# Kernel optimization log

Measured on AMD Instinct MI355X. Metric: run time of the kernel, lower is better.

The kernel has to match this reference:

```python
import jax, jax.numpy as jnp
import numpy as np

B, D = 16384, 1024
H1, H2 = 512, 256
T = 3          # num_tasks
E_SH = 2       # num_shared_experts
E_SP = 2       # num_specific_experts
G = E_SH + E_SP


def setup_inputs() -> dict:
    key = jax.random.key(0)
    ks = jax.random.split(key, 8)
    def glorot(k, shape, fan_in, fan_out):
        return jax.random.normal(k, shape, jnp.float32) * jnp.sqrt(2.0 / (fan_in + fan_out))
    return {
        "x": jax.random.normal(ks[0], (B, D), jnp.float32),
        "shared_W1": glorot(ks[1], (E_SH, D, H1), D, H1),
        "shared_b1": jnp.zeros((E_SH, H1), jnp.float32),
        "shared_W2": glorot(ks[2], (E_SH, H1, H2), H1, H2),
        "shared_b2": jnp.zeros((E_SH, H2), jnp.float32),
        "spec_W1": glorot(ks[3], (T, E_SP, D, H1), D, H1),
        "spec_b1": jnp.zeros((T, E_SP, H1), jnp.float32),
        "spec_W2": glorot(ks[4], (T, E_SP, H1, H2), H1, H2),
        "spec_b2": jnp.zeros((T, E_SP, H2), jnp.float32),
        "gate_W": glorot(ks[5], (T, D, G), D, G),
        "gate_b": jnp.zeros((T, G), jnp.float32),
    }


def reference(x, shared_W1, shared_b1, shared_W2, shared_b2,
              spec_W1, spec_b1, spec_W2, spec_b2, gate_W, gate_b):
    # Shared experts: two-layer MLP with relu, batched over experts. [B, E_SH, H2]
    sh = jax.nn.relu(jnp.einsum('bi,eih->beh', x, shared_W1) + shared_b1)
    sh = jax.nn.relu(jnp.einsum('beh,eho->beo', sh, shared_W2) + shared_b2)
    # Task-specific experts, batched over (task, expert). [B, T, E_SP, H2]
    sp = jax.nn.relu(jnp.einsum('bi,teih->bteh', x, spec_W1) + spec_b1)
    sp = jax.nn.relu(jnp.einsum('bteh,teho->bteo', sp, spec_W2) + spec_b2)
    # Gates: single linear layer per task + softmax over G=E_SH+E_SP experts. [B, T, G]
    gate = jax.nn.softmax(jnp.einsum('bi,tig->btg', x, gate_W) + gate_b, axis=-1)
    # Experts stacked in order: shared first, then specific (matches tf.stack order).
    sh_b = jnp.broadcast_to(sh[:, None], (B, T, E_SH, H2))
    experts = jnp.concatenate([sh_b, sp], axis=2)  # [B, T, G, H2]
    # Gate-weighted sum over the expert axis -> per-task outputs [B, T, H2]
    out = jnp.einsum('btgh,btg->bth', experts, gate)
    return out
```

## Files before the change

### kernel.cpp

```cpp
#include <hip/hip_runtime.h>
#include <hip/hip_bf16.h>
#include <stdint.h>

#define B_SZ 16384
#define D_SZ 1024
#define H1_SZ 512
#define H2_SZ 256
#define T_SZ 3
#define ESH 2
#define NE 8

typedef __bf16 bf16x8 __attribute__((ext_vector_type(8)));
typedef float f32x4 __attribute__((ext_vector_type(4)));
typedef unsigned short u16;
typedef u16 u16x8 __attribute__((ext_vector_type(8)));

__device__ __forceinline__ u16 f2bf(float f) {
  union { float f; uint32_t u; } v; v.f = f;
  uint32_t u = v.u;
  uint32_t r = (u + 0x7FFFu + ((u >> 16) & 1u)) >> 16;
  return (u16)r;
}
__device__ __forceinline__ float bf2f(u16 b) {
  union { uint32_t u; float f; } v; v.u = ((uint32_t)b) << 16;
  return v.f;
}

__device__ __forceinline__ void gload16(const u16* src, u16* dst_lds) {
  __builtin_amdgcn_global_load_lds(
      (const __attribute__((address_space(1))) void*)src,
      (__attribute__((address_space(3))) void*)dst_lds, 16, 0, 0);
}

__global__ __launch_bounds__(256) void cast_f32_to_bf16(
    const float* __restrict__ in, u16* __restrict__ out, int n8) {
  int i = blockIdx.x * blockDim.x + threadIdx.x;
  if (i >= n8) return;
  const float4* p = (const float4*)in + (size_t)i * 2;
  float4 a = p[0], b = p[1];
  u16x8 o;
  o[0] = f2bf(a.x); o[1] = f2bf(a.y); o[2] = f2bf(a.z); o[3] = f2bf(a.w);
  o[4] = f2bf(b.x); o[5] = f2bf(b.y); o[6] = f2bf(b.z); o[7] = f2bf(b.w);
  *((u16x8*)out + i) = o;
}

__global__ __launch_bounds__(256) void transpose_cast(
    const float* __restrict__ src, u16* __restrict__ dst, int K, int N) {
  __shared__ float tile[32][33];
  size_t e = blockIdx.z;
  const float* s = src + e * (size_t)K * N;
  u16* d = dst + e * (size_t)K * N;
  int n0 = blockIdx.x * 32, k0 = blockIdx.y * 32;
  int tx = threadIdx.x, ty = threadIdx.y;
#pragma unroll
  for (int i = ty; i < 32; i += 8)
    tile[i][tx] = s[(size_t)(k0 + i) * N + n0 + tx];
  __syncthreads();
#pragma unroll
  for (int i = ty; i < 32; i += 8)
    d[(size_t)(n0 + i) * K + k0 + tx] = f2bf(tile[tx][i]);
}

__global__ __launch_bounds__(256, 2) void gemm_ring3(
    const u16* __restrict__ A, size_t strideAe,
    const u16* __restrict__ Bt,
    const float* __restrict__ bias_sh, const float* __restrict__ bias_sp,
    u16* __restrict__ C, int M, int N, int K, int ntn_sh) {
  __shared__ __align__(16) u16 lds[3 * 12288];
  const int tid = threadIdx.x;
  const int wid = tid >> 6, lane = tid & 63;
  const int fr = lane & 15, fq = lane >> 4;
  const int wc = wid;

  const int bid = blockIdx.x;
  const int e = bid & 7;
  const int r = bid >> 3;
  const int mtile = r >> ntn_sh;
  const int ntile = r & ((1 << ntn_sh) - 1);
  const int m0 = mtile * 128, n0 = ntile * 256;

  const u16* Ae = A + (size_t)e * strideAe;
  const u16* Be = Bt + (size_t)e * (size_t)N * K;
  const int NT = K >> 5;

  const u16* pA[2];
  const u16* pB[4];
#pragma unroll
  for (int p = 0; p < 2; ++p) {
    int c = p * 256 + tid, row = c >> 2, sl = (c & 3) ^ ((row >> 1) & 3);
    pA[p] = Ae + (size_t)(m0 + row) * K + sl * 8;
  }
#pragma unroll
  for (int p = 0; p < 4; ++p) {
    int c = p * 256 + tid, row = c >> 2, sl = (c & 3) ^ ((row >> 1) & 3);
    pB[p] = Be + (size_t)(n0 + row) * K + sl * 8;
  }
  const int wdst = wid * 512;

  int offA[8], offB[4];
#pragma unroll
  for (int m = 0; m < 8; ++m) {
    int rr = m * 16 + fr;
    offA[m] = rr * 32 + ((fq ^ ((rr >> 1) & 3)) * 8);
  }
#pragma unroll
  for (int n = 0; n < 4; ++n) {
    int cg = wc * 64 + n * 16 + fr;
    offB[n] = 4096 + cg * 32 + ((fq ^ ((cg >> 1) & 3)) * 8);
  }

  f32x4 acc[8][4] = {};

#define STAGE(t, sb) do {                                             \
    gload16(pA[0] + (size_t)(t) * 32, &lds[(sb) + wdst]);             \
    gload16(pA[1] + (size_t)(t) * 32, &lds[(sb) + 2048 + wdst]);      \
    gload16(pB[0] + (size_t)(t) * 32, &lds[(sb) + 4096 + wdst]);      \
    gload16(pB[1] + (size_t)(t) * 32, &lds[(sb) + 6144 + wdst]);      \
    gload16(pB[2] + (size_t)(t) * 32, &lds[(sb) + 8192 + wdst]);      \
    gload16(pB[3] + (size_t)(t) * 32, &lds[(sb) + 10240 + wdst]); } while (0)

  STAGE(0, 0);
  STAGE(1, 12288);
  asm volatile("s_waitcnt vmcnt(6)");
  __builtin_amdgcn_s_barrier();
  __builtin_amdgcn_sched_barrier(0);

  int sb_cur = 0;
  for (int t = 0; t < NT; ++t) {
    const u16* sl = &lds[sb_cur];
    bf16x8 av[8], bv[4];
#pragma unroll
    for (int m = 0; m < 8; ++m) av[m] = *(const bf16x8*)&sl[offA[m]];
#pragma unroll
    for (int n = 0; n < 4; ++n) bv[n] = *(const bf16x8*)&sl[offB[n]];
    if (t + 2 < NT) {
      int sb_n2 = sb_cur + 2 * 12288;
      if (sb_n2 >= 36864) sb_n2 -= 36864;
      STAGE(t + 2, sb_n2);
    }
    __builtin_amdgcn_s_setprio(1);
#pragma unroll
    for (int m = 0; m < 8; ++m)
#pragma unroll
      for (int n = 0; n < 4; ++n)
        acc[m][n] = __builtin_amdgcn_mfma_f32_16x16x32_bf16(av[m], bv[n], acc[m][n], 0, 0, 0);
    __builtin_amdgcn_s_setprio(0);
    if (t + 2 < NT)      asm volatile("s_waitcnt vmcnt(6)");
    else if (t + 1 < NT) asm volatile("s_waitcnt vmcnt(0)");
    __builtin_amdgcn_s_barrier();
    __builtin_amdgcn_sched_barrier(0);
    sb_cur += 12288;
    if (sb_cur >= 36864) sb_cur = 0;
  }
#undef STAGE

  const float* bias = (e < ESH) ? (bias_sh + (size_t)e * N)
                                : (bias_sp + (size_t)(e - ESH) * N);
  u16* Ce = C + (size_t)e * (size_t)M * N;
  float bb[4];
#pragma unroll
  for (int n = 0; n < 4; ++n) bb[n] = bias[n0 + wc * 64 + n * 16 + fr];

#pragma unroll
  for (int m = 0; m < 8; ++m) {
#pragma unroll
    for (int n = 0; n < 4; ++n) {
      const int col = wc * 64 + n * 16 + fr;
      f32x4 a = acc[m][n];
#pragma unroll
      for (int rr = 0; rr < 4; ++rr) {
        float v = a[rr] + bb[n];
        v = v > 0.f ? v : 0.f;
        lds[(m * 16 + fq * 4 + rr) * 264 + col] = f2bf(v);
      }
    }
  }
  __builtin_amdgcn_s_barrier();
  const int cc = (tid & 31) * 8;
  const int rr8 = tid >> 5;
#pragma unroll
  for (int pass = 0; pass < 16; ++pass) {
    const int lr = pass * 8 + rr8;
    u16x8 vv = *(const u16x8*)&lds[lr * 264 + cc];
    *(u16x8*)&Ce[(size_t)(m0 + lr) * N + n0 + cc] = vv;
  }
}

__global__ __launch_bounds__(256) void gates_kernel(
    const float* __restrict__ x, const float* __restrict__ gW,
    const float* __restrict__ gb, float* __restrict__ gates) {
  __shared__ float gw[12][1024];
  const int tid = threadIdx.x;
  for (int i = tid; i < 12 * 1024; i += 256) {
    int tg = i >> 10, k = i & 1023;
    gw[tg][k] = gW[(size_t)(tg >> 2) * 4096 + (size_t)k * 4 + (tg & 3)];
  }
  __syncthreads();
  const int wid = tid >> 6, lane = tid & 63;
  const size_t b = (size_t)blockIdx.x * 4 + wid;
  const float* xr = x + b * 1024;
  float acc[12] = {};
  for (int kk = 0; kk < 16; ++kk) {
    float xv = xr[kk * 64 + lane];
#pragma unroll
    for (int t = 0; t < 12; ++t) acc[t] += xv * gw[t][kk * 64 + lane];
  }
#pragma unroll
  for (int off = 32; off >= 1; off >>= 1)
#pragma unroll
    for (int t = 0; t < 12; ++t) acc[t] += __shfl_xor(acc[t], off);
  if (lane == 0) {
    float* gr = gates + b * 12;
#pragma unroll
    for (int t = 0; t < 3; ++t) {
      float l0 = acc[t * 4 + 0] + gb[t * 4 + 0];
      float l1 = acc[t * 4 + 1] + gb[t * 4 + 1];
      float l2 = acc[t * 4 + 2] + gb[t * 4 + 2];
      float l3 = acc[t * 4 + 3] + gb[t * 4 + 3];
      float mx = fmaxf(fmaxf(l0, l1), fmaxf(l2, l3));
      float e0 = __expf(l0 - mx), e1 = __expf(l1 - mx);
      float e2 = __expf(l2 - mx), e3 = __expf(l3 - mx);
      float inv = 1.f / (e0 + e1 + e2 + e3);
      gr[t * 4 + 0] = e0 * inv; gr[t * 4 + 1] = e1 * inv;
      gr[t * 4 + 2] = e2 * inv; gr[t * 4 + 3] = e3 * inv;
    }
  }
}

__global__ __launch_bounds__(256) void combine_kernel(
    const u16* __restrict__ y2, const float* __restrict__ gates,
    float* __restrict__ out) {
  const int tid = threadIdx.x;
  const int rb = tid >> 5;
  const int hc = (tid & 31) * 8;
  const size_t b = (size_t)blockIdx.x * 8 + rb;
  const float* g = gates + b * 12;
  float acc0[8] = {}, acc1[8] = {}, acc2[8] = {};
#pragma unroll
  for (int e = 0; e < 8; ++e) {
    u16x8 v = *(const u16x8*)&y2[(size_t)e * B_SZ * H2_SZ + b * H2_SZ + hc];
    float f[8];
#pragma unroll
    for (int i = 0; i < 8; ++i) f[i] = bf2f(v[i]);
    if (e < 2) {
      float g0 = g[0 * 4 + e], g1 = g[1 * 4 + e], g2 = g[2 * 4 + e];
#pragma unroll
      for (int i = 0; i < 8; ++i) {
        acc0[i] += g0 * f[i]; acc1[i] += g1 * f[i]; acc2[i] += g2 * f[i];
      }
    } else {
      const int t = (e - 2) >> 1, gi = 2 + ((e - 2) & 1);
      float gv = g[t * 4 + gi];
      float* acc = (t == 0) ? acc0 : (t == 1) ? acc1 : acc2;
#pragma unroll
      for (int i = 0; i < 8; ++i) acc[i] += gv * f[i];
    }
  }
  float* o = out + b * (3 * 256);
  *(float4*)&o[0 * 256 + hc]     = make_float4(acc0[0], acc0[1], acc0[2], acc0[3]);
  *(float4*)&o[0 * 256 + hc + 4] = make_float4(acc0[4], acc0[5], acc0[6], acc0[7]);
  *(float4*)&o[1 * 256 + hc]     = make_float4(acc1[0], acc1[1], acc1[2], acc1[3]);
  *(float4*)&o[1 * 256 + hc + 4] = make_float4(acc1[4], acc1[5], acc1[6], acc1[7]);
  *(float4*)&o[2 * 256 + hc]     = make_float4(acc2[0], acc2[1], acc2[2], acc2[3]);
  *(float4*)&o[2 * 256 + hc + 4] = make_float4(acc2[4], acc2[5], acc2[6], acc2[7]);
}

extern "C" void kernel_launch(void* const* d_in, const int* in_sizes, int n_in,
                              void* d_out, int out_size, void* d_ws, size_t ws_size,
                              hipStream_t stream) {
  (void)in_sizes; (void)n_in; (void)out_size; (void)ws_size;
  const float* x   = (const float*)d_in[0];
  const float* sW1 = (const float*)d_in[1];
  const float* sb1 = (const float*)d_in[2];
  const float* sW2 = (const float*)d_in[3];
  const float* sb2 = (const float*)d_in[4];
  const float* pW1 = (const float*)d_in[5];
  const float* pb1 = (const float*)d_in[6];
  const float* pW2 = (const float*)d_in[7];
  const float* pb2 = (const float*)d_in[8];
  const float* gW  = (const float*)d_in[9];
  const float* gb  = (const float*)d_in[10];

  uint8_t* ws = (uint8_t*)d_ws;
  u16* xb    = (u16*)(ws);
  u16* w1t   = (u16*)(ws + 33554432);
  u16* w2t   = (u16*)(ws + 41943040);
  u16* y1    = (u16*)(ws + 44040192);
  u16* y2    = (u16*)(ws + 178257920);
  float* gts = (float*)(ws + 245366784);

  cast_f32_to_bf16<<<(B_SZ * D_SZ / 8 + 255) / 256, 256, 0, stream>>>(
      x, xb, B_SZ * D_SZ / 8);

  transpose_cast<<<dim3(512 / 32, 1024 / 32, 2), dim3(32, 8), 0, stream>>>(
      sW1, w1t, 1024, 512);
  transpose_cast<<<dim3(512 / 32, 1024 / 32, 6), dim3(32, 8), 0, stream>>>(
      pW1, w1t + (size_t)2 * 1024 * 512, 1024, 512);
  transpose_cast<<<dim3(256 / 32, 512 / 32, 2), dim3(32, 8), 0, stream>>>(
      sW2, w2t, 512, 256);
  transpose_cast<<<dim3(256 / 32, 512 / 32, 6), dim3(32, 8), 0, stream>>>(
      pW2, w2t + (size_t)2 * 512 * 256, 512, 256);

  gates_kernel<<<B_SZ / 4, 256, 0, stream>>>(x, gW, gb, gts);

  gemm_ring3<<<(B_SZ / 128) * (512 / 256) * NE, 256, 0, stream>>>(
      xb, 0, w1t, sb1, pb1, y1, B_SZ, 512, 1024, 1);

  gemm_ring3<<<(B_SZ / 128) * (256 / 256) * NE, 256, 0, stream>>>(
      y1, (size_t)B_SZ * 512, w2t, sb2, pb2, y2, B_SZ, 256, 512, 0);

  combine_kernel<<<B_SZ / 8, 256, 0, stream>>>(y2, gts, (float*)d_out);
}
```

Baseline: 309.1 us.

## Fuse layer-2 GEMM with gated combine; merge casts into gates and transpose kernels

Replaces the second expert GEMM and the combine kernel with a single kernel. It loops over all 8 experts for a 64x128 output tile, applies bias and ReLU, and accumulates the gate-weighted sum in registers. This avoids writing the bf16 y2 intermediate to memory and reading it back. It also folds the x cast into the gates kernel and merges the four weight transposes into one launch. The cost is fewer blocks (512) with smaller tiles, a serial loop over experts, and a large register footprint for the per-task accumulators.

```diff
diff --git a/kernel.cpp b/kernel.cpp
--- a/kernel.cpp
+++ b/kernel.cpp
@@ -32,24 +32,26 @@
       (__attribute__((address_space(3))) void*)dst_lds, 16, 0, 0);
 }
 
-__global__ __launch_bounds__(256) void cast_f32_to_bf16(
-    const float* __restrict__ in, u16* __restrict__ out, int n8) {
-  int i = blockIdx.x * blockDim.x + threadIdx.x;
-  if (i >= n8) return;
-  const float4* p = (const float4*)in + (size_t)i * 2;
-  float4 a = p[0], b = p[1];
-  u16x8 o;
-  o[0] = f2bf(a.x); o[1] = f2bf(a.y); o[2] = f2bf(a.z); o[3] = f2bf(a.w);
-  o[4] = f2bf(b.x); o[5] = f2bf(b.y); o[6] = f2bf(b.z); o[7] = f2bf(b.w);
-  *((u16x8*)out + i) = o;
-}
-
-__global__ __launch_bounds__(256) void transpose_cast(
-    const float* __restrict__ src, u16* __restrict__ dst, int K, int N) {
+__global__ __launch_bounds__(256) void transpose_cast_all(
+    const float* __restrict__ sW1, const float* __restrict__ pW1,
+    const float* __restrict__ sW2, const float* __restrict__ pW2,
+    u16* __restrict__ w1t, u16* __restrict__ w2t) {
   __shared__ float tile[32][33];
-  size_t e = blockIdx.z;
-  const float* s = src + e * (size_t)K * N;
-  u16* d = dst + e * (size_t)K * N;
+  const int z = blockIdx.z;
+  int K, N;
+  const float* s;
+  u16* d;
+  if (z < 8) {
+    K = 1024; N = 512;
+    s = (z < 2) ? (sW1 + (size_t)z * K * N) : (pW1 + (size_t)(z - 2) * K * N);
+    d = w1t + (size_t)z * K * N;
+  } else {
+    K = 512; N = 256;
+    const int e = z - 8;
+    if (blockIdx.x >= 8 || blockIdx.y >= 16) return;
+    s = (e < 2) ? (sW2 + (size_t)e * K * N) : (pW2 + (size_t)(e - 2) * K * N);
+    d = w2t + (size_t)e * K * N;
+  }
   int n0 = blockIdx.x * 32, k0 = blockIdx.y * 32;
   int tx = threadIdx.x, ty = threadIdx.y;
 #pragma unroll
@@ -61,134 +63,10 @@
     d[(size_t)(n0 + i) * K + k0 + tx] = f2bf(tile[tx][i]);
 }
 
-__global__ __launch_bounds__(256, 2) void gemm_ring3(
-    const u16* __restrict__ A, size_t strideAe,
-    const u16* __restrict__ Bt,
-    const float* __restrict__ bias_sh, const float* __restrict__ bias_sp,
-    u16* __restrict__ C, int M, int N, int K, int ntn_sh) {
-  __shared__ __align__(16) u16 lds[3 * 12288];
-  const int tid = threadIdx.x;
-  const int wid = tid >> 6, lane = tid & 63;
-  const int fr = lane & 15, fq = lane >> 4;
-  const int wc = wid;
-
-  const int bid = blockIdx.x;
-  const int e = bid & 7;
-  const int r = bid >> 3;
-  const int mtile = r >> ntn_sh;
-  const int ntile = r & ((1 << ntn_sh) - 1);
-  const int m0 = mtile * 128, n0 = ntile * 256;
-
-  const u16* Ae = A + (size_t)e * strideAe;
-  const u16* Be = Bt + (size_t)e * (size_t)N * K;
-  const int NT = K >> 5;
-
-  const u16* pA[2];
-  const u16* pB[4];
-#pragma unroll
-  for (int p = 0; p < 2; ++p) {
-    int c = p * 256 + tid, row = c >> 2, sl = (c & 3) ^ ((row >> 1) & 3);
-    pA[p] = Ae + (size_t)(m0 + row) * K + sl * 8;
-  }
-#pragma unroll
-  for (int p = 0; p < 4; ++p) {
-    int c = p * 256 + tid, row = c >> 2, sl = (c & 3) ^ ((row >> 1) & 3);
-    pB[p] = Be + (size_t)(n0 + row) * K + sl * 8;
-  }
-  const int wdst = wid * 512;
-
-  int offA[8], offB[4];
-#pragma unroll
-  for (int m = 0; m < 8; ++m) {
-    int rr = m * 16 + fr;
-    offA[m] = rr * 32 + ((fq ^ ((rr >> 1) & 3)) * 8);
-  }
-#pragma unroll
-  for (int n = 0; n < 4; ++n) {
-    int cg = wc * 64 + n * 16 + fr;
-    offB[n] = 4096 + cg * 32 + ((fq ^ ((cg >> 1) & 3)) * 8);
-  }
-
-  f32x4 acc[8][4] = {};
-
-#define STAGE(t, sb) do {                                             \
-    gload16(pA[0] + (size_t)(t) * 32, &lds[(sb) + wdst]);             \
-    gload16(pA[1] + (size_t)(t) * 32, &lds[(sb) + 2048 + wdst]);      \
-    gload16(pB[0] + (size_t)(t) * 32, &lds[(sb) + 4096 + wdst]);      \
-    gload16(pB[1] + (size_t)(t) * 32, &lds[(sb) + 6144 + wdst]);      \
-    gload16(pB[2] + (size_t)(t) * 32, &lds[(sb) + 8192 + wdst]);      \
-    gload16(pB[3] + (size_t)(t) * 32, &lds[(sb) + 10240 + wdst]); } while (0)
-
-  STAGE(0, 0);
-  STAGE(1, 12288);
-  asm volatile("s_waitcnt vmcnt(6)");
-  __builtin_amdgcn_s_barrier();
-  __builtin_amdgcn_sched_barrier(0);
-
-  int sb_cur = 0;
-  for (int t = 0; t < NT; ++t) {
-    const u16* sl = &lds[sb_cur];
-    bf16x8 av[8], bv[4];
-#pragma unroll
-    for (int m = 0; m < 8; ++m) av[m] = *(const bf16x8*)&sl[offA[m]];
-#pragma unroll
-    for (int n = 0; n < 4; ++n) bv[n] = *(const bf16x8*)&sl[offB[n]];
-    if (t + 2 < NT) {
-      int sb_n2 = sb_cur + 2 * 12288;
-      if (sb_n2 >= 36864) sb_n2 -= 36864;
-      STAGE(t + 2, sb_n2);
-    }
-    __builtin_amdgcn_s_setprio(1);
-#pragma unroll
-    for (int m = 0; m < 8; ++m)
-#pragma unroll
-      for (int n = 0; n < 4; ++n)
-        acc[m][n] = __builtin_amdgcn_mfma_f32_16x16x32_bf16(av[m], bv[n], acc[m][n], 0, 0, 0);
-    __builtin_amdgcn_s_setprio(0);
-    if (t + 2 < NT)      asm volatile("s_waitcnt vmcnt(6)");
-    else if (t + 1 < NT) asm volatile("s_waitcnt vmcnt(0)");
-    __builtin_amdgcn_s_barrier();
-    __builtin_amdgcn_sched_barrier(0);
-    sb_cur += 12288;
-    if (sb_cur >= 36864) sb_cur = 0;
-  }
-#undef STAGE
-
-  const float* bias = (e < ESH) ? (bias_sh + (size_t)e * N)
-                                : (bias_sp + (size_t)(e - ESH) * N);
-  u16* Ce = C + (size_t)e * (size_t)M * N;
-  float bb[4];
-#pragma unroll
-  for (int n = 0; n < 4; ++n) bb[n] = bias[n0 + wc * 64 + n * 16 + fr];
-
-#pragma unroll
-  for (int m = 0; m < 8; ++m) {
-#pragma unroll
-    for (int n = 0; n < 4; ++n) {
-      const int col = wc * 64 + n * 16 + fr;
-      f32x4 a = acc[m][n];
-#pragma unroll
-      for (int rr = 0; rr < 4; ++rr) {
-        float v = a[rr] + bb[n];
-        v = v > 0.f ? v : 0.f;
-        lds[(m * 16 + fq * 4 + rr) * 264 + col] = f2bf(v);
-      }
-    }
-  }
-  __builtin_amdgcn_s_barrier();
-  const int cc = (tid & 31) * 8;
-  const int rr8 = tid >> 5;
-#pragma unroll
-  for (int pass = 0; pass < 16; ++pass) {
-    const int lr = pass * 8 + rr8;
-    u16x8 vv = *(const u16x8*)&lds[lr * 264 + cc];
-    *(u16x8*)&Ce[(size_t)(m0 + lr) * N + n0 + cc] = vv;
-  }
-}
-
-__global__ __launch_bounds__(256) void gates_kernel(
+__global__ __launch_bounds__(256) void gates_cast_kernel(
     const float* __restrict__ x, const float* __restrict__ gW,
-    const float* __restrict__ gb, float* __restrict__ gates) {
+    const float* __restrict__ gb, float* __restrict__ gates,
+    u16* __restrict__ xb) {
   __shared__ float gw[12][1024];
   const int tid = threadIdx.x;
   for (int i = tid; i < 12 * 1024; i += 256) {
@@ -199,9 +77,11 @@
   const int wid = tid >> 6, lane = tid & 63;
   const size_t b = (size_t)blockIdx.x * 4 + wid;
   const float* xr = x + b * 1024;
+  u16* xbr = xb + b * 1024;
   float acc[12] = {};
   for (int kk = 0; kk < 16; ++kk) {
     float xv = xr[kk * 64 + lane];
+    xbr[kk * 64 + lane] = f2bf(xv);
 #pragma unroll
     for (int t = 0; t < 12; ++t) acc[t] += xv * gw[t][kk * 64 + lane];
   }
@@ -227,42 +107,271 @@
   }
 }
 
-__global__ __launch_bounds__(256) void combine_kernel(
-    const u16* __restrict__ y2, const float* __restrict__ gates,
-    float* __restrict__ out) {
+__global__ __launch_bounds__(256, 2) void gemm_ring3(
+    const u16* __restrict__ A, size_t strideAe,
+    const u16* __restrict__ Bt,
+    const float* __restrict__ bias_sh, const float* __restrict__ bias_sp,
+    u16* __restrict__ C, int M, int N, int K, int ntn_sh) {
+  __shared__ __align__(16) u16 lds[3 * 12288];
   const int tid = threadIdx.x;
-  const int rb = tid >> 5;
-  const int hc = (tid & 31) * 8;
-  const size_t b = (size_t)blockIdx.x * 8 + rb;
-  const float* g = gates + b * 12;
-  float acc0[8] = {}, acc1[8] = {}, acc2[8] = {};
-#pragma unroll
-  for (int e = 0; e < 8; ++e) {
-    u16x8 v = *(const u16x8*)&y2[(size_t)e * B_SZ * H2_SZ + b * H2_SZ + hc];
-    float f[8];
-#pragma unroll
-    for (int i = 0; i < 8; ++i) f[i] = bf2f(v[i]);
-    if (e < 2) {
-      float g0 = g[0 * 4 + e], g1 = g[1 * 4 + e], g2 = g[2 * 4 + e];
-#pragma unroll
-      for (int i = 0; i < 8; ++i) {
-        acc0[i] += g0 * f[i]; acc1[i] += g1 * f[i]; acc2[i] += g2 * f[i];
+  const int wid = tid >> 6, lane = tid & 63;
+  const int fr = lane & 15, fq = lane >> 4;
+  const int wc = wid;
+
+  const int bid = blockIdx.x;
+  const int e = bid & 7;
+  const int r = bid >> 3;
+  const int mtile = r >> ntn_sh;
+  const int ntile = r & ((1 << ntn_sh) - 1);
+  const int m0 = mtile * 128, n0 = ntile * 256;
+
+  const u16* Ae = A + (size_t)e * strideAe;
+  const u16* Be = Bt + (size_t)e * (size_t)N * K;
+  const int NT = K >> 5;
+
+  const u16* pA[2];
+  const u16* pB[4];
+#pragma unroll
+  for (int p = 0; p < 2; ++p) {
+    int c = p * 256 + tid, row = c >> 2, sl = (c & 3) ^ ((row >> 1) & 3);
+    pA[p] = Ae + (size_t)(m0 + row) * K + sl * 8;
+  }
+#pragma unroll
+  for (int p = 0; p < 4; ++p) {
+    int c = p * 256 + tid, row = c >> 2, sl = (c & 3) ^ ((row >> 1) & 3);
+    pB[p] = Be + (size_t)(n0 + row) * K + sl * 8;
+  }
+  const int wdst = wid * 512;
+
+  int offA[8], offB[4];
+#pragma unroll
+  for (int m = 0; m < 8; ++m) {
+    int rr = m * 16 + fr;
+    offA[m] = rr * 32 + ((fq ^ ((rr >> 1) & 3)) * 8);
+  }
+#pragma unroll
+  for (int n = 0; n < 4; ++n) {
+    int cg = wc * 64 + n * 16 + fr;
+    offB[n] = 4096 + cg * 32 + ((fq ^ ((cg >> 1) & 3)) * 8);
+  }
+
+  f32x4 acc[8][4] = {};
+
+#define STAGE(t, sb) do {                                             \
+    gload16(pA[0] + (size_t)(t) * 32, &lds[(sb) + wdst]);             \
+    gload16(pA[1] + (size_t)(t) * 32, &lds[(sb) + 2048 + wdst]);      \
+    gload16(pB[0] + (size_t)(t) * 32, &lds[(sb) + 4096 + wdst]);      \
+    gload16(pB[1] + (size_t)(t) * 32, &lds[(sb) + 6144 + wdst]);      \
+    gload16(pB[2] + (size_t)(t) * 32, &lds[(sb) + 8192 + wdst]);      \
+    gload16(pB[3] + (size_t)(t) * 32, &lds[(sb) + 10240 + wdst]); } while (0)
+
+  STAGE(0, 0);
+  STAGE(1, 12288);
+  asm volatile("s_waitcnt vmcnt(6)");
+  __builtin_amdgcn_s_barrier();
+  __builtin_amdgcn_sched_barrier(0);
+
+  int sb_cur = 0;
+  for (int t = 0; t < NT; ++t) {
+    const u16* sl = &lds[sb_cur];
+    bf16x8 av[8], bv[4];
+#pragma unroll
+    for (int m = 0; m < 8; ++m) av[m] = *(const bf16x8*)&sl[offA[m]];
+#pragma unroll
+    for (int n = 0; n < 4; ++n) bv[n] = *(const bf16x8*)&sl[offB[n]];
+    if (t + 2 < NT) {
+      int sb_n2 = sb_cur + 2 * 12288;
+      if (sb_n2 >= 36864) sb_n2 -= 36864;
+      STAGE(t + 2, sb_n2);
+    }
+    __builtin_amdgcn_s_setprio(1);
+#pragma unroll
+    for (int m = 0; m < 8; ++m)
+#pragma unroll
+      for (int n = 0; n < 4; ++n)
+        acc[m][n] = __builtin_amdgcn_mfma_f32_16x16x32_bf16(av[m], bv[n], acc[m][n], 0, 0, 0);
+    __builtin_amdgcn_s_setprio(0);
+    if (t + 2 < NT)      asm volatile("s_waitcnt vmcnt(6)");
+    else if (t + 1 < NT) asm volatile("s_waitcnt vmcnt(0)");
+    __builtin_amdgcn_s_barrier();
+    __builtin_amdgcn_sched_barrier(0);
+    sb_cur += 12288;
+    if (sb_cur >= 36864) sb_cur = 0;
+  }
+#undef STAGE
+
+  const float* bias = (e < ESH) ? (bias_sh + (size_t)e * N)
+                                : (bias_sp + (size_t)(e - ESH) * N);
+  u16* Ce = C + (size_t)e * (size_t)M * N;
+  float bb[4];
+#pragma unroll
+  for (int n = 0; n < 4; ++n) bb[n] = bias[n0 + wc * 64 + n * 16 + fr];
+
+#pragma unroll
+  for (int m = 0; m < 8; ++m) {
+#pragma unroll
+    for (int n = 0; n < 4; ++n) {
+      const int col = wc * 64 + n * 16 + fr;
+      f32x4 a = acc[m][n];
+#pragma unroll
+      for (int rr = 0; rr < 4; ++rr) {
+        float v = a[rr] + bb[n];
+        v = v > 0.f ? v : 0.f;
+        lds[(m * 16 + fq * 4 + rr) * 264 + col] = f2bf(v);
       }
-    } else {
-      const int t = (e - 2) >> 1, gi = 2 + ((e - 2) & 1);
-      float gv = g[t * 4 + gi];
-      float* acc = (t == 0) ? acc0 : (t == 1) ? acc1 : acc2;
-#pragma unroll
-      for (int i = 0; i < 8; ++i) acc[i] += gv * f[i];
     }
   }
-  float* o = out + b * (3 * 256);
-  *(float4*)&o[0 * 256 + hc]     = make_float4(acc0[0], acc0[1], acc0[2], acc0[3]);
-  *(float4*)&o[0 * 256 + hc + 4] = make_float4(acc0[4], acc0[5], acc0[6], acc0[7]);
-  *(float4*)&o[1 * 256 + hc]     = make_float4(acc1[0], acc1[1], acc1[2], acc1[3]);
-  *(float4*)&o[1 * 256 + hc + 4] = make_float4(acc1[4], acc1[5], acc1[6], acc1[7]);
-  *(float4*)&o[2 * 256 + hc]     = make_float4(acc2[0], acc2[1], acc2[2], acc2[3]);
-  *(float4*)&o[2 * 256 + hc + 4] = make_float4(acc2[4], acc2[5], acc2[6], acc2[7]);
+  __builtin_amdgcn_s_barrier();
+  const int cc = (tid & 31) * 8;
+  const int rr8 = tid >> 5;
+#pragma unroll
+  for (int pass = 0; pass < 16; ++pass) {
+    const int lr = pass * 8 + rr8;
+    u16x8 vv = *(const u16x8*)&lds[lr * 264 + cc];
+    *(u16x8*)&Ce[(size_t)(m0 + lr) * N + n0 + cc] = vv;
+  }
+}
+
+__global__ __launch_bounds__(256, 2) void fused_l2c(
+    const u16* __restrict__ y1, const u16* __restrict__ w2t,
+    const float* __restrict__ sb2, const float* __restrict__ pb2,
+    const float* __restrict__ gts, float* __restrict__ out) {
+  __shared__ __align__(16) u16 ring[3 * 6144];
+  __shared__ float gl[64 * 12];
+  __shared__ float bl[8 * 128];
+  const int tid = threadIdx.x;
+  const int wid = tid >> 6, lane = tid & 63;
+  const int fr = lane & 15, fq = lane >> 4;
+
+  const int bid = blockIdx.x;
+  const int bm = bid >> 1, bn = bid & 1;
+  const int m0 = bm * 64;
+  const int ncol0 = bn * 128;
+
+  for (int i = tid; i < 768; i += 256)
+    gl[i] = gts[(size_t)(m0 + i / 12) * 12 + (i % 12)];
+  for (int i = tid; i < 1024; i += 256) {
+    int e = i >> 7, c = i & 127;
+    bl[i] = (e < 2) ? sb2[e * 256 + ncol0 + c] : pb2[(e - 2) * 256 + ncol0 + c];
+  }
+
+  const int cA = tid, rowA = cA >> 2, slA = (cA & 3) ^ ((rowA >> 1) & 3);
+  const u16* pAf = y1 + (size_t)(m0 + rowA) * 512 + slA * 8;
+  const u16* pBf[2];
+#pragma unroll
+  for (int p = 0; p < 2; ++p) {
+    int c = p * 256 + tid, row = c >> 2, sl = (c & 3) ^ ((row >> 1) & 3);
+    pBf[p] = w2t + (size_t)(ncol0 + row) * 512 + sl * 8;
+  }
+  const int wdst = wid * 512;
+
+  int offA[4], offB[2];
+#pragma unroll
+  for (int m = 0; m < 4; ++m) {
+    int rr = m * 16 + fr;
+    offA[m] = rr * 32 + ((fq ^ ((rr >> 1) & 3)) * 8);
+  }
+#pragma unroll
+  for (int n = 0; n < 2; ++n) {
+    int cg = wid * 32 + n * 16 + fr;
+    offB[n] = 2048 + cg * 32 + ((fq ^ ((cg >> 1) & 3)) * 8);
+  }
+
+  f32x4 acc[4][2] = {};
+  float oa[3][4][2][4] = {};
+
+#define STAGE2(g, sb) do {                                                      \
+    const size_t eo = (size_t)((g) >> 4);                                       \
+    const int ko = ((g) & 15) * 32;                                             \
+    gload16(pAf + eo * ((size_t)B_SZ * 512) + ko, &ring[(sb) + wdst]);          \
+    gload16(pBf[0] + eo * 131072 + ko, &ring[(sb) + 2048 + wdst]);              \
+    gload16(pBf[1] + eo * 131072 + ko, &ring[(sb) + 4096 + wdst]); } while (0)
+
+  STAGE2(0, 0);
+  STAGE2(1, 6144);
+  __syncthreads();
+
+  int sb_cur = 0;
+  for (int g = 0; g < 128; ++g) {
+    const u16* sl = &ring[sb_cur];
+    bf16x8 av[4], bv[2];
+#pragma unroll
+    for (int m = 0; m < 4; ++m) av[m] = *(const bf16x8*)&sl[offA[m]];
+#pragma unroll
+    for (int n = 0; n < 2; ++n) bv[n] = *(const bf16x8*)&sl[offB[n]];
+    if (g + 2 < 128) {
+      int sb_n2 = sb_cur + 2 * 6144;
+      if (sb_n2 >= 18432) sb_n2 -= 18432;
+      STAGE2(g + 2, sb_n2);
+    }
+    __builtin_amdgcn_s_setprio(1);
+#pragma unroll
+    for (int m = 0; m < 4; ++m)
+#pragma unroll
+      for (int n = 0; n < 2; ++n)
+        acc[m][n] = __builtin_amdgcn_mfma_f32_16x16x32_bf16(av[m], bv[n], acc[m][n], 0, 0, 0);
+    __builtin_amdgcn_s_setprio(0);
+    if (g + 2 < 128)      asm volatile("s_waitcnt vmcnt(3)");
+    else if (g + 1 < 128) asm volatile("s_waitcnt vmcnt(0)");
+    __builtin_amdgcn_s_barrier();
+    __builtin_amdgcn_sched_barrier(0);
+    sb_cur += 6144;
+    if (sb_cur >= 18432) sb_cur = 0;
+
+    if ((g & 15) == 15) {
+      const int e = g >> 4;
+#pragma unroll
+      for (int m = 0; m < 4; ++m) {
+#pragma unroll
+        for (int rr = 0; rr < 4; ++rr) {
+          const int row = m * 16 + fq * 4 + rr;
+          if (e < 2) {
+            const float g0 = gl[row * 12 + 0 * 4 + e];
+            const float g1 = gl[row * 12 + 1 * 4 + e];
+            const float g2 = gl[row * 12 + 2 * 4 + e];
+#pragma unroll
+            for (int n = 0; n < 2; ++n) {
+              const int col = wid * 32 + n * 16 + fr;
+              float v = acc[m][n][rr] + bl[e * 128 + col];
+              v = v > 0.f ? v : 0.f;
+              oa[0][m][n][rr] += g0 * v;
+              oa[1][m][n][rr] += g1 * v;
+              oa[2][m][n][rr] += g2 * v;
+            }
+          } else {
+            const int t = (e - 2) >> 1, gi = 2 + ((e - 2) & 1);
+            const float gv = gl[row * 12 + t * 4 + gi];
+#pragma unroll
+            for (int n = 0; n < 2; ++n) {
+              const int col = wid * 32 + n * 16 + fr;
+              float v = acc[m][n][rr] + bl[e * 128 + col];
+              v = v > 0.f ? v : 0.f;
+              if (t == 0) oa[0][m][n][rr] += gv * v;
+              else if (t == 1) oa[1][m][n][rr] += gv * v;
+              else oa[2][m][n][rr] += gv * v;
+            }
+          }
+#pragma unroll
+          for (int n = 0; n < 2; ++n) acc[m][n][rr] = 0.f;
+        }
+      }
+    }
+  }
+#undef STAGE2
+
+#pragma unroll
+  for (int t = 0; t < 3; ++t)
+#pragma unroll
+    for (int m = 0; m < 4; ++m)
+#pragma unroll
+      for (int rr = 0; rr < 4; ++rr) {
+        const int row = m * 16 + fq * 4 + rr;
+#pragma unroll
+        for (int n = 0; n < 2; ++n) {
+          const int col = wid * 32 + n * 16 + fr;
+          out[(size_t)(m0 + row) * 768 + t * 256 + ncol0 + col] = oa[t][m][n][rr];
+        }
+      }
 }
 
 extern "C" void kernel_launch(void* const* d_in, const int* in_sizes, int n_in,
@@ -286,28 +395,16 @@
   u16* w1t   = (u16*)(ws + 33554432);
   u16* w2t   = (u16*)(ws + 41943040);
   u16* y1    = (u16*)(ws + 44040192);
-  u16* y2    = (u16*)(ws + 178257920);
-  float* gts = (float*)(ws + 245366784);
-
-  cast_f32_to_bf16<<<(B_SZ * D_SZ / 8 + 255) / 256, 256, 0, stream>>>(
-      x, xb, B_SZ * D_SZ / 8);
-
-  transpose_cast<<<dim3(512 / 32, 1024 / 32, 2), dim3(32, 8), 0, stream>>>(
-      sW1, w1t, 1024, 512);
-  transpose_cast<<<dim3(512 / 32, 1024 / 32, 6), dim3(32, 8), 0, stream>>>(
-      pW1, w1t + (size_t)2 * 1024 * 512, 1024, 512);
-  transpose_cast<<<dim3(256 / 32, 512 / 32, 2), dim3(32, 8), 0, stream>>>(
-      sW2, w2t, 512, 256);
-  transpose_cast<<<dim3(256 / 32, 512 / 32, 6), dim3(32, 8), 0, stream>>>(
-      pW2, w2t + (size_t)2 * 512 * 256, 512, 256);
-
-  gates_kernel<<<B_SZ / 4, 256, 0, stream>>>(x, gW, gb, gts);
+  float* gts = (float*)(ws + 178257920);
+
+  transpose_cast_all<<<dim3(16, 32, 16), dim3(32, 8), 0, stream>>>(
+      sW1, pW1, sW2, pW2, w1t, w2t);
+
+  gates_cast_kernel<<<B_SZ / 4, 256, 0, stream>>>(x, gW, gb, gts, xb);
 
   gemm_ring3<<<(B_SZ / 128) * (512 / 256) * NE, 256, 0, stream>>>(
       xb, 0, w1t, sb1, pb1, y1, B_SZ, 512, 1024, 1);
 
-  gemm_ring3<<<(B_SZ / 128) * (256 / 256) * NE, 256, 0, stream>>>(
-      y1, (size_t)B_SZ * 512, w2t, sb2, pb2, y2, B_SZ, 256, 512, 0);
-
-  combine_kernel<<<B_SZ / 8, 256, 0, stream>>>(y2, gts, (float*)d_out);
-}
+  fused_l2c<<<(B_SZ / 64) * 2, 256, 0, stream>>>(
+      y1, w2t, sb2, pb2, gts, (float*)d_out);
+}
```

After: 322.8 us. 1.04x slower.
